# Performance work log

Measured on AMD Instinct MI355X. Metric: run time of the kernel, lower is better.

## Reference

```python
import jax, jax.numpy as jnp
import numpy as np

BATCH, N, M, DIM, HID = 4, 2048, 2048, 128, 128
TB = 64  # target block size (mirrors the torch blocked loop, bounds the ijh intermediate)


def setup_inputs() -> dict:
    key = jax.random.key(0)
    k0, k1, k2, k3, k4, k5 = jax.random.split(key, 6)
    s_in = 1.0 / np.sqrt(DIM)
    s_out = 1.0 / np.sqrt(HID)
    return {
        "target_val": jax.random.normal(k0, (BATCH, N, DIM), jnp.float32),
        "source_val": jax.random.normal(k1, (BATCH, M, DIM), jnp.float32),
        "W_in": jax.random.uniform(k2, (HID, DIM), jnp.float32, -s_in, s_in),
        "b_in": jax.random.uniform(k3, (HID,), jnp.float32, -s_in, s_in),
        "W_out": jax.random.uniform(k4, (1, HID), jnp.float32, -s_out, s_out),
        "b_out": jax.random.uniform(k5, (1,), jnp.float32, -s_out, s_out),
    }


def reference(target_val, source_val, W_in, b_in, W_out, b_out):
    # out[b,i,j] = W_out @ silu(W_in @ (t_i * s_j) + b_in) + b_out
    B, Nt, d = target_val.shape
    nb = Nt // TB
    w_out = W_out[0]  # [HID]
    # [nb, B, TB, d] so we can scan over target blocks without materializing [B,N,M,HID]
    t_blocks = target_val.reshape(B, nb, TB, d).transpose(1, 0, 2, 3)

    def block_fn(t_chunk):  # t_chunk: [B, TB, d]
        hidden = jnp.einsum('bid,hd,bjd->bijh', t_chunk, W_in, source_val)  # [B,TB,M,HID]
        hidden = jax.nn.silu(hidden + b_in)
        return jnp.einsum('bijh,h->bij', hidden, w_out) + b_out[0]  # [B,TB,M]

    out_blocks = jax.lax.map(block_fn, t_blocks)  # [nb, B, TB, M]
    return out_blocks.transpose(1, 0, 2, 3).reshape(B, Nt, M)
```

## Files before the change

kernel.cpp:

```cpp
#include <hip/hip_runtime.h>

#define BATCH 4
#define NN 2048
#define MM 2048
#define DIM 128
#define HID 128

typedef __bf16 bf16x8 __attribute__((ext_vector_type(8)));
typedef float f32x16 __attribute__((ext_vector_type(16)));
typedef float f32x4 __attribute__((ext_vector_type(4)));
typedef float f32x2 __attribute__((ext_vector_type(2)));
typedef unsigned short ushort_t;
typedef ushort_t ushort8 __attribute__((ext_vector_type(8)));
typedef unsigned int uint_t;

#define LOG2E 1.44269504088896340736f
#define LN2   0.69314718055994530942f

__device__ __forceinline__ ushort_t f2bf(float f) {
  uint_t u = __builtin_bit_cast(uint_t, f);
  u += 0x7fffu + ((u >> 16) & 1u);
  return (ushort_t)(u >> 16);
}
__device__ __forceinline__ float bflo(uint_t p) { return __builtin_bit_cast(float, p << 16); }
__device__ __forceinline__ float bfhi(uint_t p) { return __builtin_bit_cast(float, p & 0xffff0000u); }

__global__ void cvt_repack(const float* __restrict__ src, ushort_t* __restrict__ dst) {
  int t = blockIdx.x * 256 + threadIdx.x;
  int c    = t & 63;
  int ks   = (t >> 6) & 7;
  int jt   = (t >> 9) & 63;
  int b    = t >> 15;
  int half = c >> 5, l5 = c & 31;
  int j    = jt * 32 + l5;
  int d0   = ks * 16 + half * 8;
  const float* s = src + ((size_t)(b * MM + j)) * DIM + d0;
  float4 v0 = *reinterpret_cast<const float4*>(s);
  float4 v1 = *reinterpret_cast<const float4*>(s + 4);
  ushort8 u;
  u[0] = f2bf(v0.x); u[1] = f2bf(v0.y); u[2] = f2bf(v0.z); u[3] = f2bf(v0.w);
  u[4] = f2bf(v1.x); u[5] = f2bf(v1.y); u[6] = f2bf(v1.z); u[7] = f2bf(v1.w);
  *reinterpret_cast<ushort8*>(dst + (size_t)t * 8) = u;
}

__global__ void pbw_kernel(const float* __restrict__ b_in, const float* __restrict__ w_out,
                           uint_t* __restrict__ pbw) {
  int h = threadIdx.x;
  pbw[h] = (uint_t)f2bf(b_in[h] * LOG2E) | ((uint_t)f2bf(w_out[h] * LN2) << 16);
}

__launch_bounds__(256, 3)
__global__ void hmlp_kernel(const float* __restrict__ Tg, const ushort_t* __restrict__ Sb,
                            const float* __restrict__ Wg, const uint_t* __restrict__ pbw,
                            const float* __restrict__ b_out_p, float* __restrict__ Og) {
  __shared__ float part[4][MM];
  __shared__ ushort_t Bst[2][4096];
  const int tid  = threadIdx.x;
  const int lane = tid & 63;
  const int wv   = tid >> 6;
  const int half = lane >> 5;
  const int l5   = lane & 31;
  const int blk  = blockIdx.x;
  const int b    = blk >> 11;
  const int i    = blk & 2047;
  const int hb   = wv << 5;

  f32x16 cinit;
  f32x2 w2[8];
#pragma unroll
  for (int r = 0; r < 16; ++r) {
    uint_t pw = pbw[hb + (r & 3) + 8 * (r >> 2) + 4 * half];
    cinit[r] = bflo(pw);
    if (r & 1) w2[r >> 1].y = bfhi(pw); else w2[r >> 1].x = bfhi(pw);
  }

  bf16x8 afr[8];
  {
    const float* tb = Tg + ((size_t)(b * NN + i)) * DIM;
    const float* wr = Wg + (size_t)(hb + l5) * DIM;
#pragma unroll
    for (int ks = 0; ks < 8; ++ks) {
      const int d0 = ks * 16 + half * 8;
      float4 w0 = *reinterpret_cast<const float4*>(wr + d0);
      float4 w1 = *reinterpret_cast<const float4*>(wr + d0 + 4);
      float4 t0 = *reinterpret_cast<const float4*>(tb + d0);
      float4 t1 = *reinterpret_cast<const float4*>(tb + d0 + 4);
      ushort8 u;
      u[0] = f2bf(w0.x * t0.x * LOG2E); u[1] = f2bf(w0.y * t0.y * LOG2E);
      u[2] = f2bf(w0.z * t0.z * LOG2E); u[3] = f2bf(w0.w * t0.w * LOG2E);
      u[4] = f2bf(w1.x * t1.x * LOG2E); u[5] = f2bf(w1.y * t1.y * LOG2E);
      u[6] = f2bf(w1.z * t1.z * LOG2E); u[7] = f2bf(w1.w * t1.w * LOG2E);
      afr[ks] = __builtin_bit_cast(bf16x8, u);
    }
  }

  const ushort_t* stage_base = Sb + (size_t)b * (64 * 4096);

  auto stage_async = [&](int jt, int buf) {
    const ushort_t* g0 = stage_base + (size_t)jt * 4096 + wv * 1024 + lane * 8;
    ushort_t* l0 = &Bst[buf][wv * 1024];
    __builtin_amdgcn_global_load_lds(
        (const __attribute__((address_space(1))) uint_t*)(g0),
        (__attribute__((address_space(3))) uint_t*)(l0), 16, 0, 0);
    __builtin_amdgcn_global_load_lds(
        (const __attribute__((address_space(1))) uint_t*)(g0 + 512),
        (__attribute__((address_space(3))) uint_t*)(l0 + 512), 16, 0, 0);
  };

  auto compute = [&](int buf, int jt) {
    const ushort_t* fb = &Bst[buf][lane * 8];
    bf16x8 B0 = *reinterpret_cast<const bf16x8*>(fb);
    bf16x8 B4 = *reinterpret_cast<const bf16x8*>(fb + 4 * 512);
    f32x16 c0 = __builtin_amdgcn_mfma_f32_32x32x16_bf16(afr[0], B0, cinit, 0, 0, 0);
    f32x16 c1 = __builtin_amdgcn_mfma_f32_32x32x16_bf16(afr[4], B4, (f32x16)(0.f), 0, 0, 0);
#pragma unroll
    for (int ks = 1; ks < 4; ++ks) {
      bf16x8 Ba = *reinterpret_cast<const bf16x8*>(fb + ks * 512);
      bf16x8 Bb = *reinterpret_cast<const bf16x8*>(fb + (ks + 4) * 512);
      c0 = __builtin_amdgcn_mfma_f32_32x32x16_bf16(afr[ks], Ba, c0, 0, 0, 0);
      c1 = __builtin_amdgcn_mfma_f32_32x32x16_bf16(afr[ks + 4], Bb, c1, 0, 0, 0);
    }

    f32x2 pc[4] = {f32x2{0.f, 0.f}, f32x2{0.f, 0.f}, f32x2{0.f, 0.f}, f32x2{0.f, 0.f}};
#define EPI_Q(q)                                                                     \
    {                                                                                \
      f32x2 y = __builtin_shufflevector(c0, c0, 2 * (q), 2 * (q) + 1)                \
              + __builtin_shufflevector(c1, c1, 2 * (q), 2 * (q) + 1);               \
      float e0 = __builtin_amdgcn_exp2f(-y.x);                                       \
      float e1 = __builtin_amdgcn_exp2f(-y.y);                                       \
      f32x2 d = f32x2{e0, e1} + 1.0f;                                                \
      f32x2 s = f32x2{__builtin_amdgcn_rcpf(d.x), __builtin_amdgcn_rcpf(d.y)};       \
      f32x2 ys = y * s;                                                              \
      pc[(q) & 3] = __builtin_elementwise_fma(w2[(q)], ys, pc[(q) & 3]);             \
    }
    EPI_Q(0) EPI_Q(1) EPI_Q(2) EPI_Q(3) EPI_Q(4) EPI_Q(5) EPI_Q(6) EPI_Q(7)
#undef EPI_Q
    f32x2 pv = (pc[0] + pc[1]) + (pc[2] + pc[3]);
    float p = pv.x + pv.y;
    p += __shfl_xor(p, 32, 64);
    if (lane < 32) part[wv][jt * 32 + l5] = p;
  };

  stage_async(0, 0);
  __syncthreads();

#pragma unroll 1
  for (int jt = 0; jt < 64; ++jt) {
    const int buf = jt & 1;
    if (jt + 1 < 64) stage_async(jt + 1, buf ^ 1);
    compute(buf, jt);
    __syncthreads();
  }

  {
    const float bo = b_out_p[0];
    const size_t ob = ((size_t)(b * NN + i)) * MM;
#pragma unroll
    for (int k = 0; k < 2; ++k) {
      const int j0 = k * 1024 + tid * 4;
      f32x4 v0 = *reinterpret_cast<const f32x4*>(&part[0][j0]);
      f32x4 v1 = *reinterpret_cast<const f32x4*>(&part[1][j0]);
      f32x4 v2 = *reinterpret_cast<const f32x4*>(&part[2][j0]);
      f32x4 v3 = *reinterpret_cast<const f32x4*>(&part[3][j0]);
      f32x4 o = (v0 + v1) + (v2 + v3);
      o[0] += bo; o[1] += bo; o[2] += bo; o[3] += bo;
      *reinterpret_cast<f32x4*>(&Og[ob + j0]) = o;
    }
  }
}

extern "C" void kernel_launch(void* const* d_in, const int* in_sizes, int n_in,
                              void* d_out, int out_size, void* d_ws, size_t ws_size,
                              hipStream_t stream) {
  const float* Tg    = (const float*)d_in[0];
  const float* Sg    = (const float*)d_in[1];
  const float* Wg    = (const float*)d_in[2];
  const float* b_in  = (const float*)d_in[3];
  const float* W_out = (const float*)d_in[4];
  const float* b_out = (const float*)d_in[5];
  float* Og = (float*)d_out;

  ushort_t* Sb = (ushort_t*)d_ws;
  uint_t* pbw  = (uint_t*)((char*)d_ws + (size_t)BATCH * MM * DIM * 2);

  cvt_repack<<<(BATCH * MM * DIM) / (256 * 8), 256, 0, stream>>>(Sg, Sb);
  pbw_kernel<<<1, 128, 0, stream>>>(b_in, W_out, pbw);
  hmlp_kernel<<<BATCH * NN, 256, 0, stream>>>(Tg, Sb, Wg, pbw, b_out, Og);
}
```

Measured before the change: 793.4 us.

## Halve partial-sum LDS buffer and use single MFMA accumulator to raise occupancy

The per-block partial-sum shared buffer is cut from the full 2048 columns to 1024 and flushed to global memory halfway through the source loop, which lowers LDS use per block. The two interleaved MFMA accumulator chains become a single chain of 8 dependent MFMAs, freeing 16 registers. Together these let the launch bound ask for 4 blocks per CU instead of 3. The cost is a serial MFMA dependency chain with less instruction-level parallelism, plus an extra barrier and store phase mid-loop.

```diff
diff --git a/kernel.cpp b/kernel.cpp
--- a/kernel.cpp
+++ b/kernel.cpp
@@ -49,11 +49,11 @@
   pbw[h] = (uint_t)f2bf(b_in[h] * LOG2E) | ((uint_t)f2bf(w_out[h] * LN2) << 16);
 }
 
-__launch_bounds__(256, 3)
+__launch_bounds__(256, 4)
 __global__ void hmlp_kernel(const float* __restrict__ Tg, const ushort_t* __restrict__ Sb,
                             const float* __restrict__ Wg, const uint_t* __restrict__ pbw,
                             const float* __restrict__ b_out_p, float* __restrict__ Og) {
-  __shared__ float part[4][MM];
+  __shared__ float part[4][1024];
   __shared__ ushort_t Bst[2][4096];
   const int tid  = threadIdx.x;
   const int lane = tid & 63;
@@ -107,25 +107,29 @@
         (__attribute__((address_space(3))) uint_t*)(l0 + 512), 16, 0, 0);
   };
 
-  auto compute = [&](int buf, int jt) {
+  const float bo = b_out_p[0];
+  const size_t ob = ((size_t)(b * NN + i)) * MM;
+
+  stage_async(0, 0);
+  __syncthreads();
+
+#pragma unroll 1
+  for (int jt = 0; jt < 64; ++jt) {
+    const int buf = jt & 1;
+    if (jt + 1 < 64) stage_async(jt + 1, buf ^ 1);
+
     const ushort_t* fb = &Bst[buf][lane * 8];
-    bf16x8 B0 = *reinterpret_cast<const bf16x8*>(fb);
-    bf16x8 B4 = *reinterpret_cast<const bf16x8*>(fb + 4 * 512);
-    f32x16 c0 = __builtin_amdgcn_mfma_f32_32x32x16_bf16(afr[0], B0, cinit, 0, 0, 0);
-    f32x16 c1 = __builtin_amdgcn_mfma_f32_32x32x16_bf16(afr[4], B4, (f32x16)(0.f), 0, 0, 0);
+    f32x16 c = __builtin_amdgcn_mfma_f32_32x32x16_bf16(
+        afr[0], *reinterpret_cast<const bf16x8*>(fb), cinit, 0, 0, 0);
 #pragma unroll
-    for (int ks = 1; ks < 4; ++ks) {
-      bf16x8 Ba = *reinterpret_cast<const bf16x8*>(fb + ks * 512);
-      bf16x8 Bb = *reinterpret_cast<const bf16x8*>(fb + (ks + 4) * 512);
-      c0 = __builtin_amdgcn_mfma_f32_32x32x16_bf16(afr[ks], Ba, c0, 0, 0, 0);
-      c1 = __builtin_amdgcn_mfma_f32_32x32x16_bf16(afr[ks + 4], Bb, c1, 0, 0, 0);
-    }
+    for (int ks = 1; ks < 8; ++ks)
+      c = __builtin_amdgcn_mfma_f32_32x32x16_bf16(
+          afr[ks], *reinterpret_cast<const bf16x8*>(fb + ks * 512), c, 0, 0, 0);
 
     f32x2 pc[4] = {f32x2{0.f, 0.f}, f32x2{0.f, 0.f}, f32x2{0.f, 0.f}, f32x2{0.f, 0.f}};
 #define EPI_Q(q)                                                                     \
     {                                                                                \
-      f32x2 y = __builtin_shufflevector(c0, c0, 2 * (q), 2 * (q) + 1)                \
-              + __builtin_shufflevector(c1, c1, 2 * (q), 2 * (q) + 1);               \
+      f32x2 y = __builtin_shufflevector(c, c, 2 * (q), 2 * (q) + 1);                 \
       float e0 = __builtin_amdgcn_exp2f(-y.x);                                       \
       float e1 = __builtin_amdgcn_exp2f(-y.y);                                       \
       f32x2 d = f32x2{e0, e1} + 1.0f;                                                \
@@ -138,33 +142,21 @@
     f32x2 pv = (pc[0] + pc[1]) + (pc[2] + pc[3]);
     float p = pv.x + pv.y;
     p += __shfl_xor(p, 32, 64);
-    if (lane < 32) part[wv][jt * 32 + l5] = p;
-  };
+    if (lane < 32) part[wv][(jt & 31) * 32 + l5] = p;
 
-  stage_async(0, 0);
-  __syncthreads();
+    __syncthreads();
 
-#pragma unroll 1
-  for (int jt = 0; jt < 64; ++jt) {
-    const int buf = jt & 1;
-    if (jt + 1 < 64) stage_async(jt + 1, buf ^ 1);
-    compute(buf, jt);
-    __syncthreads();
-  }
-
-  {
-    const float bo = b_out_p[0];
-    const size_t ob = ((size_t)(b * NN + i)) * MM;
-#pragma unroll
-    for (int k = 0; k < 2; ++k) {
-      const int j0 = k * 1024 + tid * 4;
+    if ((jt & 31) == 31) {
+      const int phase = jt >> 5;
+      const int j0 = tid * 4;
       f32x4 v0 = *reinterpret_cast<const f32x4*>(&part[0][j0]);
       f32x4 v1 = *reinterpret_cast<const f32x4*>(&part[1][j0]);
       f32x4 v2 = *reinterpret_cast<const f32x4*>(&part[2][j0]);
       f32x4 v3 = *reinterpret_cast<const f32x4*>(&part[3][j0]);
       f32x4 o = (v0 + v1) + (v2 + v3);
       o[0] += bo; o[1] += bo; o[2] += bo; o[3] += bo;
-      *reinterpret_cast<f32x4*>(&Og[ob + j0]) = o;
+      *reinterpret_cast<f32x4*>(&Og[ob + phase * 1024 + j0]) = o;
+      __syncthreads();
     }
   }
 }
```

After: 737.1 us. -7.1%, faster.
